# Optimization experiments

Hardware: AMD Instinct MI355X
Metric: run time of the kernel (lower is better)

Reference implementation:

```python
import jax, jax.numpy as jnp
import numpy as np

B, S, H, NH = 2, 2048, 768, 12
HD = H // NH
MEM_W = 0.5  # memory_weight
LN_EPS = 1e-5


def setup_inputs() -> dict:
    key = jax.random.key(0)
    ks = jax.random.split(key, 12)
    xav = lambda k: jax.random.uniform(k, (H, H), jnp.float32, -1.0, 1.0) * np.sqrt(6.0 / (H + H))
    return {
        "hidden_states": jax.random.normal(ks[0], (B, S, H), jnp.float32),
        "cross_states": jax.random.normal(ks[1], (B, S, H), jnp.float32),
        "attention_mask": jnp.ones((B, 1, S, S), jnp.int32),
        "memory_tensors": jax.random.normal(ks[2], (2, B, S, H), jnp.float32),
        "dynamic_factor": jax.random.uniform(ks[3], (B, S, 1), jnp.float32),
        "Wq": xav(ks[4]), "bq": jnp.zeros((H,), jnp.float32),
        "Wk": xav(ks[5]), "bk": jnp.zeros((H,), jnp.float32),
        "Wv": xav(ks[6]), "bv": jnp.zeros((H,), jnp.float32),
        "Wo": xav(ks[7]), "bo": jnp.zeros((H,), jnp.float32),
        "gate": jnp.ones((1,), jnp.float32),
        "gate_bias": jnp.zeros((1,), jnp.float32),
        "ln_g": jnp.ones((H,), jnp.float32),
        "ln_b": jnp.zeros((H,), jnp.float32),
    }


def _layernorm(x, g, b):
    mu = jnp.mean(x, axis=-1, keepdims=True)
    var = jnp.mean(jnp.square(x - mu), axis=-1, keepdims=True)
    return (x - mu) * jax.lax.rsqrt(var + LN_EPS) * g + b


def reference(hidden_states, cross_states, attention_mask, memory_tensors,
              dynamic_factor, Wq, bq, Wk, bk, Wv, bv, Wo, bo,
              gate, gate_bias, ln_g, ln_b):
    x = _layernorm(hidden_states, ln_g, ln_b)
    q = x @ Wq + bq                      # [B,S,H]
    k = cross_states @ Wk + bk
    v = cross_states @ Wv + bv
    k = k + memory_tensors[0] * MEM_W    # memory injection into K/V
    v = v + memory_tensors[1] * MEM_W

    q = q.reshape(B, S, NH, HD).transpose(0, 2, 1, 3)  # [B,NH,S,HD]
    k = k.reshape(B, S, NH, HD).transpose(0, 2, 1, 3)
    v = v.reshape(B, S, NH, HD).transpose(0, 2, 1, 3)

    scores = jnp.einsum("bhqd,bhkd->bhqk", q, k) / np.sqrt(HD)
    scores = jnp.where(attention_mask == 0, -jnp.inf, scores)
    attn = jax.nn.softmax(scores, axis=-1)
    out = jnp.einsum("bhqk,bhkd->bhqd", attn, v)       # [B,NH,S,HD]
    out = out.transpose(0, 2, 1, 3).reshape(B, S, H)

    out = out @ Wo + bo
    out = out * gate + gate_bias
    out = out * dynamic_factor
    return out
```

## Files before the change

kernel.cpp:

```cpp
#include <hip/hip_runtime.h>
#include <hip/hip_bf16.h>
#include <stdint.h>

#define BB   2
#define SS   2048
#define HH   768
#define NHH  12
#define HDD  64
#define BSS  (BB*SS)
#define NBH  (BB*NHH)
#define ROWS_BH (NBH*SS)
#define NSPLIT 2

typedef unsigned short u16;
typedef unsigned int   u32;
typedef __attribute__((ext_vector_type(8))) short bf16x8_t;
typedef __attribute__((ext_vector_type(4))) float f32x4;
typedef __attribute__((ext_vector_type(2))) u32   u32x2;
typedef __attribute__((ext_vector_type(4))) u32   u32x4;

#define MFMA16(a, b, c) __builtin_amdgcn_mfma_f32_16x16x32_bf16((a), (b), (c), 0, 0, 0)

__device__ __forceinline__ float b2f(u16 u) {
    u32 x = ((u32)u) << 16; float f; __builtin_memcpy(&f, &x, 4); return f;
}
__device__ __forceinline__ u16 f2b(float f) {
    u32 x; __builtin_memcpy(&x, &f, 4);
    u32 r = x + 0x7fffu + ((x >> 16) & 1u);
    return (u16)(r >> 16);
}
__device__ __forceinline__ void async16(const u16* g, u16* l) {
    __builtin_amdgcn_global_load_lds(
        (const __attribute__((address_space(1))) void*)g,
        (__attribute__((address_space(3))) void*)l, 16, 0, 0);
}

__global__ __launch_bounds__(256) void prep_kernel(
    const float* __restrict__ Wq, const float* __restrict__ Wk,
    const float* __restrict__ Wv, const float* __restrict__ Wo,
    u16* __restrict__ Wt,
    const float* __restrict__ hid, const float* __restrict__ cross,
    const float* __restrict__ g, const float* __restrict__ bb,
    u16* __restrict__ xln, u16* __restrict__ crossb,
    const int* __restrict__ mask, u32* __restrict__ bits,
    u32* __restrict__ wrow)
{
    int id = blockIdx.x;
    int t = threadIdx.x;

    if (id < 576) {
        int mat = id / 144, rem = id % 144;
        int by = rem / 12, bx = rem % 12;
        const float* src = (mat == 0) ? Wq : (mat == 1) ? Wk : (mat == 2) ? Wv : Wo;
        u16* dst = Wt + (size_t)mat * 768 * 768;

        __shared__ float sm[64][68];
        int r0 = by * 64, c0 = bx * 64;
        #pragma unroll
        for (int it = 0; it < 4; ++it) {
            int c = t + it * 256;
            int r = c >> 4, sg = c & 15;
            *(float4*)&sm[r][sg * 4] = *(const float4*)&src[(size_t)(r0 + r) * 768 + c0 + sg * 4];
        }
        __syncthreads();
        #pragma unroll
        for (int it = 0; it < 2; ++it) {
            int c = t + it * 256;
            int rr = c >> 3, sg = c & 7;
            u16 tmp[8] __attribute__((aligned(16)));
            #pragma unroll
            for (int j = 0; j < 8; ++j) tmp[j] = f2b(sm[sg * 8 + j][rr]);
            *(u32x4*)&dst[(size_t)(c0 + rr) * 768 + r0 + sg * 8] = *(u32x4*)tmp;
        }
        return;
    }

    if (id < 2624) {
        int lid = id - 576;
        int y = lid >> 10, bx = lid & 1023;
        int wv = t >> 6, lane = t & 63;
        int row = bx * 4 + wv;

        if (y == 1) {
            const float* xr = cross + (size_t)row * 768;
            u16* o = crossb + (size_t)row * 768;
            #pragma unroll
            for (int c = 0; c < 3; ++c) {
                float4 f = *(const float4*)&xr[c * 256 + lane * 4];
                u16 t4[4] __attribute__((aligned(8)));
                t4[0] = f2b(f.x); t4[1] = f2b(f.y); t4[2] = f2b(f.z); t4[3] = f2b(f.w);
                *(u32x2*)&o[c * 256 + lane * 4] = *(u32x2*)t4;
            }
            return;
        }

        const float* xr = hid + (size_t)row * 768;
        float v[12];
        float s = 0.f, s2 = 0.f;
        #pragma unroll
        for (int c = 0; c < 3; ++c) {
            float4 f = *(const float4*)&xr[c * 256 + lane * 4];
            v[c*4+0] = f.x; v[c*4+1] = f.y; v[c*4+2] = f.z; v[c*4+3] = f.w;
            s  += f.x + f.y + f.z + f.w;
            s2 += f.x*f.x + f.y*f.y + f.z*f.z + f.w*f.w;
        }
        #pragma unroll
        for (int off = 1; off < 64; off <<= 1) {
            s  += __shfl_xor(s,  off, 64);
            s2 += __shfl_xor(s2, off, 64);
        }
        float mu  = s  * (1.f / 768.f);
        float var = s2 * (1.f / 768.f) - mu * mu;
        float rs  = 1.f / sqrtf(var + 1e-5f);
        #pragma unroll
        for (int c = 0; c < 3; ++c) {
            float4 gg = *(const float4*)&g [c * 256 + lane * 4];
            float4 bv = *(const float4*)&bb[c * 256 + lane * 4];
            u16 o[4] __attribute__((aligned(8)));
            o[0] = f2b((v[c*4+0] - mu) * rs * gg.x + bv.x);
            o[1] = f2b((v[c*4+1] - mu) * rs * gg.y + bv.y);
            o[2] = f2b((v[c*4+2] - mu) * rs * gg.z + bv.z);
            o[3] = f2b((v[c*4+3] - mu) * rs * gg.w + bv.w);
            *(u32x2*)&xln[(size_t)row * 768 + c * 256 + lane * 4] = *(u32x2*)o;
        }
        return;
    }

    {
        int mid = id - 2624;
        int w = mid * 256 + t;
        const int4* p = (const int4*)(mask + (size_t)w * 32);
        u32 v = 0;
        #pragma unroll
        for (int i = 0; i < 8; ++i) {
            int4 m = p[i];
            v |= ((m.x != 0) ? 1u : 0u) << (4 * i + 0);
            v |= ((m.y != 0) ? 1u : 0u) << (4 * i + 1);
            v |= ((m.z != 0) ? 1u : 0u) << (4 * i + 2);
            v |= ((m.w != 0) ? 1u : 0u) << (4 * i + 3);
        }
        bits[w] = v;
        unsigned long long ball = __ballot(v == 0xffffffffu);
        if ((t & 63) == 0) {
            u32 wr = 0;
            #pragma unroll
            for (int kt = 0; kt < 32; ++kt)
                if (((ball >> (2 * kt)) & 3ull) == 3ull) wr |= (1u << kt);
            wrow[w >> 6] = wr;
        }
    }
}

__device__ __forceinline__ void gemm64_main(const u16* __restrict__ A,
                                            const u16* __restrict__ W,
                                            f32x4 acc[2][4])
{
    __shared__ __attribute__((aligned(16))) u16 AsL[64 * 64];
    __shared__ __attribute__((aligned(16))) u16 BsL[128 * 64];
    int m0 = blockIdx.x * 64, n0 = blockIdx.y * 128;
    int t = threadIdx.x;
    int wv = t >> 6, lane = t & 63, lm = lane & 15, quad = lane >> 4;
    int wr = wv >> 1, wc = wv & 1;

    for (int kt = 0; kt < 768 / 64; ++kt) {
        __syncthreads();
        #pragma unroll
        for (int it = 0; it < 2; ++it) {
            int c = t + it * 256;
            int row = c >> 3, cs = (c & 7) ^ (row & 7);
            async16(A + (size_t)(m0 + row) * 768 + kt * 64 + cs * 8, &AsL[c * 8]);
        }
        #pragma unroll
        for (int it = 0; it < 4; ++it) {
            int c = t + it * 256;
            int row = c >> 3, cs = (c & 7) ^ (row & 7);
            async16(W + (size_t)(n0 + row) * 768 + kt * 64 + cs * 8, &BsL[c * 8]);
        }
        __syncthreads();
        #pragma unroll
        for (int kk = 0; kk < 2; ++kk) {
            bf16x8_t af[2], bfv[4];
            #pragma unroll
            for (int i = 0; i < 2; ++i) {
                int r = wr * 32 + i * 16 + lm;
                af[i] = *(const bf16x8_t*)&AsL[(r * 8 + ((kk * 4 + quad) ^ (r & 7))) * 8];
            }
            #pragma unroll
            for (int j = 0; j < 4; ++j) {
                int r = wc * 64 + j * 16 + lm;
                bfv[j] = *(const bf16x8_t*)&BsL[(r * 8 + ((kk * 4 + quad) ^ (r & 7))) * 8];
            }
            #pragma unroll
            for (int i = 0; i < 2; ++i)
                #pragma unroll
                for (int j = 0; j < 4; ++j)
                    acc[i][j] = MFMA16(af[i], bfv[j], acc[i][j]);
        }
    }
}

__global__ __launch_bounds__(256) void qkv_gemm(
    const u16* __restrict__ xln, const u16* __restrict__ crossb,
    const u16* __restrict__ Wt,  const float* __restrict__ bq,
    const float* __restrict__ bk, const float* __restrict__ bv,
    const float* __restrict__ mem,
    u16* __restrict__ Qb, u16* __restrict__ Kb, u16* __restrict__ VtG)
{
    int z = blockIdx.z;
    const u16* A      = (z == 0) ? xln : crossb;
    const u16* W      = Wt + (size_t)z * 768 * 768;
    const float* bias = (z == 0) ? bq : (z == 1) ? bk : bv;
    const float* mp   = (z == 0) ? (const float*)nullptr : mem + (size_t)(z - 1) * BSS * HH;

    f32x4 z4 = {0.f, 0.f, 0.f, 0.f};
    f32x4 acc[2][4];
    #pragma unroll
    for (int i = 0; i < 2; ++i)
        #pragma unroll
        for (int j = 0; j < 4; ++j) acc[i][j] = z4;

    gemm64_main(A, W, acc);

    int t = threadIdx.x, wv = t >> 6, lane = t & 63, lm = lane & 15, quad = lane >> 4;
    int wr = wv >> 1, wc = wv & 1;
    int row0 = blockIdx.x * 64 + wr * 32 + quad * 4;
    int col0 = blockIdx.y * 128 + wc * 64 + lm;

    if (z == 2) {
        #pragma unroll
        for (int j = 0; j < 4; ++j) {
            int cg = col0 + j * 16;
            float bz = bias[cg];
            int h = cg >> 6, d = cg & 63;
            #pragma unroll
            for (int i = 0; i < 2; ++i) {
                int rg = row0 + i * 16;
                int b = rg >> 11, s = rg & 2047;
                u16 ob[4] __attribute__((aligned(8)));
                #pragma unroll
                for (int e = 0; e < 4; ++e) {
                    float v = acc[i][j][e] + bz + 0.5f * mp[(size_t)(rg + e) * HH + cg];
                    ob[e] = f2b(v);
                }
                *(u32x2*)&VtG[((size_t)(b * NHH + h) * 64 + d) * SS + s] = *(u32x2*)ob;
            }
        }
        return;
    }

    u16* out = (z == 0) ? Qb : Kb;
    #pragma unroll
    for (int j = 0; j < 4; ++j) {
        int cg = col0 + j * 16;
        float bz = bias[cg];
        #pragma unroll
        for (int i = 0; i < 2; ++i) {
            int rg = row0 + i * 16;
            #pragma unroll
            for (int e = 0; e < 4; ++e) {
                float v = acc[i][j][e] + bz;
                if (mp) v += 0.5f * mp[(size_t)(rg + e) * HH + cg];
                out[(size_t)(rg + e) * HH + cg] = f2b(v);
            }
        }
    }
}

__global__ __launch_bounds__(512) void attn_kernel(
    const u16* __restrict__ Q, const u16* __restrict__ K,
    const u16* __restrict__ VtG, const u32* __restrict__ mbits,
    const u32* __restrict__ wrow,
    u16* __restrict__ Pacc, float* __restrict__ Pl, int ksteps)
{
    __shared__ __attribute__((aligned(16))) u16   KsL[2][64 * 64];
    __shared__ __attribute__((aligned(16))) u16   VtL[2][64 * 64];
    __shared__ __attribute__((aligned(16))) short Ps[8][16][72];

    int qt = blockIdx.x;
    int bh = blockIdx.y;
    int z  = blockIdx.z;
    int b = bh / NHH, h = bh % NHH;
    int t = threadIdx.x;
    int wv = t >> 6, lane = t & 63, lm = lane & 15, quad = lane >> 4;
    int r7 = lm & 7;

    int qrow_g = b * SS + qt * 128 + wv * 16;
    const u16* qp = Q + (size_t)(qrow_g + lm) * HH + h * 64;
    bf16x8_t qf0 = *(const bf16x8_t*)&qp[quad * 8];
    bf16x8_t qf1 = *(const bf16x8_t*)&qp[32 + quad * 8];

    f32x4 z4 = {0.f, 0.f, 0.f, 0.f};
    f32x4 acc_o[4] = {z4, z4, z4, z4};
    float l_part[4] = {0.f, 0.f, 0.f, 0.f};

    const float SC = 0.18033688011112042f;
    int qloc = qt * 128 + wv * 16 + quad * 4;

    u32 wand = wrow[b * SS + qloc + 0] & wrow[b * SS + qloc + 1] &
               wrow[b * SS + qloc + 2] & wrow[b * SS + qloc + 3];

    int kr = t >> 3, cs = (t & 7) ^ (kr & 7);
    const u16* Kb0 = K + (size_t)(b * SS) * HH + h * 64;
    const u16* Vb0 = VtG + (size_t)bh * 64 * SS;

    auto STAGE = [&](int pp, int kt) {
        int k0 = kt * 64;
        async16(Kb0 + (size_t)(k0 + kr) * HH + cs * 8, &KsL[pp][t * 8]);
        async16(Vb0 + (size_t)kr * SS + k0 + cs * 8,   &VtL[pp][t * 8]);
    };

    int kt0 = z * ksteps, ktE = kt0 + ksteps;
    STAGE(0, kt0);
    __syncthreads();

    for (int kt = kt0; kt < ktE; ++kt) {
        int p = (kt - kt0) & 1;
        if (kt + 1 < ktE) STAGE(p ^ 1, kt + 1);

        f32x4 sc[4];
        #pragma unroll
        for (int k16 = 0; k16 < 4; ++k16) {
            int rowk = k16 * 16 + lm;
            bf16x8_t kf0 = *(const bf16x8_t*)&KsL[p][(rowk * 8 + (quad ^ r7)) * 8];
            bf16x8_t kf1 = *(const bf16x8_t*)&KsL[p][(rowk * 8 + ((quad ^ 4) ^ r7)) * 8];
            f32x4 a = z4;
            a = MFMA16(qf0, kf0, a);
            a = MFMA16(qf1, kf1, a);
            sc[k16] = a;
        }

        if (!__all((int)((wand >> kt) & 1u))) {
            #pragma unroll
            for (int e = 0; e < 4; ++e) {
                u32x2 u = *(const u32x2*)&mbits[(size_t)(b * SS + qloc + e) * (SS / 32) + kt * 2];
                unsigned long long mw = ((unsigned long long)u.y << 32) | (unsigned long long)u.x;
                #pragma unroll
                for (int k16 = 0; k16 < 4; ++k16)
                    if (!((mw >> (k16 * 16 + lm)) & 1ull)) sc[k16][e] = -3.0e38f;
            }
        }

        #pragma unroll
        for (int k16 = 0; k16 < 4; ++k16) {
            #pragma unroll
            for (int e = 0; e < 4; ++e) {
                float pv = __builtin_amdgcn_exp2f(sc[k16][e] * SC);
                sc[k16][e] = pv;
                l_part[e] += pv;
            }
        }

        #pragma unroll
        for (int k16 = 0; k16 < 4; ++k16) {
            int colg = ((k16 + quad) & 3) * 16;
            #pragma unroll
            for (int e = 0; e < 4; ++e) {
                float pv = sc[k16][e];
                u32 pb = __builtin_bit_cast(u32, pv);
                Ps[wv][quad * 4 + e][colg + lm] = (short)((pb + 0x8000u) >> 16);
            }
        }
        __asm__ volatile("" ::: "memory");

        #pragma unroll
        for (int cc = 0; cc < 2; ++cc) {
            int k16r = cc * 2 + (quad >> 1);
            int colg = ((k16r + (lm >> 2)) & 3) * 16 + (quad & 1) * 8;
            bf16x8_t pf = *(const bf16x8_t*)&Ps[wv][lm][colg];
            #pragma unroll
            for (int j = 0; j < 4; ++j) {
                bf16x8_t vf = *(const bf16x8_t*)&VtL[p][((j * 16 + lm) * 8 + ((cc * 4 + quad) ^ r7)) * 8];
                acc_o[j] = MFMA16(pf, vf, acc_o[j]);
            }
        }

        __syncthreads();
    }

    #pragma unroll
    for (int off = 1; off < 16; off <<= 1) {
        #pragma unroll
        for (int e = 0; e < 4; ++e)
            l_part[e] += __shfl_xor(l_part[e], off, 64);
    }

    size_t prow = ((size_t)z * NBH + bh) * SS + qt * 128 + wv * 16 + quad * 4;
    #pragma unroll
    for (int j = 0; j < 4; ++j)
        #pragma unroll
        for (int e = 0; e < 4; ++e)
            Pacc[(prow + e) * 64 + j * 16 + lm] = f2b(acc_o[j][e]);
    if (lm == 0) {
        #pragma unroll
        for (int e = 0; e < 4; ++e)
            Pl[prow + e] = l_part[e];
    }
}

__global__ __launch_bounds__(256) void attn_merge(
    const u16* __restrict__ Pacc, const float* __restrict__ Pl,
    u16* __restrict__ AO)
{
    int t = threadIdx.x;
    int r = blockIdx.x * 64 + (t >> 2);
    int dseg = (t & 3) * 16;

    float lsum = Pl[r] + Pl[(size_t)ROWS_BH + r];

    float o[16];
    #pragma unroll
    for (int i = 0; i < 16; ++i) o[i] = 0.f;
    #pragma unroll
    for (int s = 0; s < NSPLIT; ++s) {
        const u16* ap = &Pacc[((size_t)s * ROWS_BH + r) * 64 + dseg];
        u32x4 a0 = *(const u32x4*)ap;
        u32x4 a1 = *(const u32x4*)(ap + 8);
        u32 wa[8];
        wa[0]=a0.x; wa[1]=a0.y; wa[2]=a0.z; wa[3]=a0.w;
        wa[4]=a1.x; wa[5]=a1.y; wa[6]=a1.z; wa[7]=a1.w;
        #pragma unroll
        for (int i = 0; i < 8; ++i) {
            o[2*i]   += b2f((u16)(wa[i] & 0xffff));
            o[2*i+1] += b2f((u16)(wa[i] >> 16));
        }
    }
    float inv = 1.f / lsum;
    int bh = r >> 11, q = r & 2047;
    int b = bh / NHH, h = bh % NHH;
    u16 ob[16] __attribute__((aligned(16)));
    #pragma unroll
    for (int i = 0; i < 16; ++i) ob[i] = f2b(o[i] * inv);
    u16* op = &AO[((size_t)(b * SS + q)) * HH + h * 64 + dseg];
    *(u32x4*)op       = *(u32x4*)ob;
    *(u32x4*)(op + 8) = *(u32x4*)(ob + 8);
}

__global__ __launch_bounds__(256) void out_gemm(
    const u16* __restrict__ AO, const u16* __restrict__ Wt,
    const float* __restrict__ bo, const float* __restrict__ gate,
    const float* __restrict__ gbias, const float* __restrict__ dyn,
    float* __restrict__ out)
{
    f32x4 z4 = {0.f, 0.f, 0.f, 0.f};
    f32x4 acc[2][4];
    #pragma unroll
    for (int i = 0; i < 2; ++i)
        #pragma unroll
        for (int j = 0; j < 4; ++j) acc[i][j] = z4;

    gemm64_main(AO, Wt, acc);

    float gv = gate[0];
    float gb = gbias[0];
    int t = threadIdx.x, wv = t >> 6, lane = t & 63, lm = lane & 15, quad = lane >> 4;
    int wr = wv >> 1, wc = wv & 1;
    int row0 = blockIdx.x * 64 + wr * 32 + quad * 4;
    int col0 = blockIdx.y * 128 + wc * 64 + lm;
    #pragma unroll
    for (int j = 0; j < 4; ++j) {
        int cg = col0 + j * 16;
        float bz = bo[cg];
        #pragma unroll
        for (int i = 0; i < 2; ++i) {
            int rg = row0 + i * 16;
            #pragma unroll
            for (int e = 0; e < 4; ++e) {
                float v = acc[i][j][e] + bz;
                v = v * gv + gb;
                v *= dyn[rg + e];
                out[(size_t)(rg + e) * HH + cg] = v;
            }
        }
    }
}

extern "C" void kernel_launch(void* const* d_in, const int* in_sizes, int n_in,
                              void* d_out, int out_size, void* d_ws, size_t ws_size,
                              hipStream_t stream)
{
    (void)in_sizes; (void)n_in; (void)out_size; (void)ws_size;

    const float* hid   = (const float*)d_in[0];
    const float* cross = (const float*)d_in[1];
    const int*   amask = (const int*)d_in[2];
    const float* mem   = (const float*)d_in[3];
    const float* dyn   = (const float*)d_in[4];
    const float* Wq    = (const float*)d_in[5];
    const float* bq    = (const float*)d_in[6];
    const float* Wk    = (const float*)d_in[7];
    const float* bk    = (const float*)d_in[8];
    const float* Wv    = (const float*)d_in[9];
    const float* bv    = (const float*)d_in[10];
    const float* Wo    = (const float*)d_in[11];
    const float* bo    = (const float*)d_in[12];
    const float* gate  = (const float*)d_in[13];
    const float* gbias = (const float*)d_in[14];
    const float* lng   = (const float*)d_in[15];
    const float* lnb   = (const float*)d_in[16];

    char* p = (char*)d_ws;
    u16* Wt   = (u16*)p; p += (size_t)4 * 768 * 768 * 2;
    u32* mb   = (u32*)p; p += (size_t)BB * SS * (SS / 32) * 4;
    u32* wrow = (u32*)p; p += (size_t)BSS * 4;
    u16* xln  = (u16*)p; p += (size_t)BSS * HH * 2;
    u16* crb  = (u16*)p; p += (size_t)BSS * HH * 2;
    u16* Qb   = (u16*)p; p += (size_t)BSS * HH * 2;
    u16* Kb   = (u16*)p; p += (size_t)BSS * HH * 2;
    u16* VtG  = (u16*)p; p += (size_t)BSS * HH * 2;
    u16* Pacc  = xln;
    float* Pl  = (float*)Wt;
    u16* AO    = Kb;

    prep_kernel <<<dim3(3648),           256, 0, stream>>>(
        Wq, Wk, Wv, Wo, Wt, hid, cross, lng, lnb, xln, crb, amask, mb, wrow);
    qkv_gemm    <<<dim3(64, 6, 3),       256, 0, stream>>>(
        xln, crb, Wt, bq, bk, bv, mem, Qb, Kb, VtG);
    attn_kernel <<<dim3(16, 24, NSPLIT), 512, 0, stream>>>(
        Qb, Kb, VtG, mb, wrow, Pacc, Pl, SS / 64 / NSPLIT);
    attn_merge  <<<dim3(ROWS_BH / 64),   256, 0, stream>>>(Pacc, Pl, AO);
    out_gemm    <<<dim3(64, 6),          256, 0, stream>>>(
        AO, Wt + (size_t)3 * 768 * 768, bo, gate, gbias, dyn, (float*)d_out);
}
```

Measured before the change: 246.3 us.

## Process two 16-row query tiles per wave in attention, halving block size

The attention kernel now uses 256 threads (4 waves), and each wave handles 32 query rows as two 16-row MFMA tiles instead of one. Each K and V fragment read from LDS is reused for two MFMAs, which cuts LDS read traffic per FLOP. The staging loop copies two chunks per thread to fill the same 64x64 tiles. The cost is roughly double the accumulator and score registers per thread; the launch bound asks for 3 blocks per CU to keep occupancy.

```diff
diff --git a/kernel.cpp b/kernel.cpp
--- a/kernel.cpp
+++ b/kernel.cpp
@@ -266,7 +266,7 @@
     }
 }
 
-__global__ __launch_bounds__(512) void attn_kernel(
+__global__ __launch_bounds__(256, 3) void attn_kernel(
     const u16* __restrict__ Q, const u16* __restrict__ K,
     const u16* __restrict__ VtG, const u32* __restrict__ mbits,
     const u32* __restrict__ wrow,
@@ -274,7 +274,7 @@
 {
     __shared__ __attribute__((aligned(16))) u16   KsL[2][64 * 64];
     __shared__ __attribute__((aligned(16))) u16   VtL[2][64 * 64];
-    __shared__ __attribute__((aligned(16))) short Ps[8][16][72];
+    __shared__ __attribute__((aligned(16))) short Ps[4][32][72];
 
     int qt = blockIdx.x;
     int bh = blockIdx.y;
@@ -284,29 +284,42 @@
     int wv = t >> 6, lane = t & 63, lm = lane & 15, quad = lane >> 4;
     int r7 = lm & 7;
 
-    int qrow_g = b * SS + qt * 128 + wv * 16;
-    const u16* qp = Q + (size_t)(qrow_g + lm) * HH + h * 64;
-    bf16x8_t qf0 = *(const bf16x8_t*)&qp[quad * 8];
-    bf16x8_t qf1 = *(const bf16x8_t*)&qp[32 + quad * 8];
+    int qrow0 = b * SS + qt * 128 + wv * 32;
+    const u16* qp0 = Q + (size_t)(qrow0 + lm) * HH + h * 64;
+    const u16* qp1 = Q + (size_t)(qrow0 + 16 + lm) * HH + h * 64;
+    bf16x8_t qa0 = *(const bf16x8_t*)&qp0[quad * 8];
+    bf16x8_t qa1 = *(const bf16x8_t*)&qp0[32 + quad * 8];
+    bf16x8_t qb0 = *(const bf16x8_t*)&qp1[quad * 8];
+    bf16x8_t qb1 = *(const bf16x8_t*)&qp1[32 + quad * 8];
 
     f32x4 z4 = {0.f, 0.f, 0.f, 0.f};
-    f32x4 acc_o[4] = {z4, z4, z4, z4};
-    float l_part[4] = {0.f, 0.f, 0.f, 0.f};
+    f32x4 acc0[4] = {z4, z4, z4, z4};
+    f32x4 acc1[4] = {z4, z4, z4, z4};
+    float l0[4] = {0.f, 0.f, 0.f, 0.f};
+    float l1[4] = {0.f, 0.f, 0.f, 0.f};
 
     const float SC = 0.18033688011112042f;
-    int qloc = qt * 128 + wv * 16 + quad * 4;
-
-    u32 wand = wrow[b * SS + qloc + 0] & wrow[b * SS + qloc + 1] &
-               wrow[b * SS + qloc + 2] & wrow[b * SS + qloc + 3];
-
-    int kr = t >> 3, cs = (t & 7) ^ (kr & 7);
+    int ql0 = qt * 128 + wv * 32 + quad * 4;
+    int ql1 = ql0 + 16;
+
+    u32 wand0 = wrow[b * SS + ql0 + 0] & wrow[b * SS + ql0 + 1] &
+                wrow[b * SS + ql0 + 2] & wrow[b * SS + ql0 + 3];
+    u32 wand1 = wrow[b * SS + ql1 + 0] & wrow[b * SS + ql1 + 1] &
+                wrow[b * SS + ql1 + 2] & wrow[b * SS + ql1 + 3];
+    u32 wandA = wand0 & wand1;
+
     const u16* Kb0 = K + (size_t)(b * SS) * HH + h * 64;
     const u16* Vb0 = VtG + (size_t)bh * 64 * SS;
 
     auto STAGE = [&](int pp, int kt) {
         int k0 = kt * 64;
-        async16(Kb0 + (size_t)(k0 + kr) * HH + cs * 8, &KsL[pp][t * 8]);
-        async16(Vb0 + (size_t)kr * SS + k0 + cs * 8,   &VtL[pp][t * 8]);
+        #pragma unroll
+        for (int it = 0; it < 2; ++it) {
+            int c = t + it * 256;
+            int kr = c >> 3, cs = (c & 7) ^ (kr & 7);
+            async16(Kb0 + (size_t)(k0 + kr) * HH + cs * 8, &KsL[pp][c * 8]);
+            async16(Vb0 + (size_t)kr * SS + k0 + cs * 8,   &VtL[pp][c * 8]);
+        }
     };
 
     int kt0 = z * ksteps, ktE = kt0 + ksteps;
@@ -317,36 +330,33 @@
         int p = (kt - kt0) & 1;
         if (kt + 1 < ktE) STAGE(p ^ 1, kt + 1);
 
-        f32x4 sc[4];
+        f32x4 sc0[4], sc1[4];
         #pragma unroll
         for (int k16 = 0; k16 < 4; ++k16) {
             int rowk = k16 * 16 + lm;
             bf16x8_t kf0 = *(const bf16x8_t*)&KsL[p][(rowk * 8 + (quad ^ r7)) * 8];
             bf16x8_t kf1 = *(const bf16x8_t*)&KsL[p][(rowk * 8 + ((quad ^ 4) ^ r7)) * 8];
-            f32x4 a = z4;
-            a = MFMA16(qf0, kf0, a);
-            a = MFMA16(qf1, kf1, a);
-            sc[k16] = a;
-        }
-
-        if (!__all((int)((wand >> kt) & 1u))) {
+            f32x4 a0 = z4, a1 = z4;
+            a0 = MFMA16(qa0, kf0, a0);
+            a1 = MFMA16(qb0, kf0, a1);
+            a0 = MFMA16(qa1, kf1, a0);
+            a1 = MFMA16(qb1, kf1, a1);
+            sc0[k16] = a0;
+            sc1[k16] = a1;
+        }
+
+        if (!__all((int)((wandA >> kt) & 1u))) {
             #pragma unroll
             for (int e = 0; e < 4; ++e) {
-                u32x2 u = *(const u32x2*)&mbits[(size_t)(b * SS + qloc + e) * (SS / 32) + kt * 2];
-                unsigned long long mw = ((unsigned long long)u.y << 32) | (unsigned long long)u.x;
+                u32x2 u0 = *(const u32x2*)&mbits[(size_t)(b * SS + ql0 + e) * (SS / 32) + kt * 2];
+                unsigned long long mw0 = ((unsigned long long)u0.y << 32) | (unsigned long long)u0.x;
+                u32x2 u1 = *(const u32x2*)&mbits[(size_t)(b * SS + ql1 + e) * (SS / 32) + kt * 2];
+                unsigned long long mw1 = ((unsigned long long)u1.y << 32) | (unsigned long long)u1.x;
                 #pragma unroll
-                for (int k16 = 0; k16 < 4; ++k16)
-                    if (!((mw >> (k16 * 16 + lm)) & 1ull)) sc[k16][e] = -3.0e38f;
-            }
-        }
-
-        #pragma unroll
-        for (int k16 = 0; k16 < 4; ++k16) {
-            #pragma unroll
-            for (int e = 0; e < 4; ++e) {
-                float pv = __builtin_amdgcn_exp2f(sc[k16][e] * SC);
-                sc[k16][e] = pv;
-                l_part[e] += pv;
+                for (int k16 = 0; k16 < 4; ++k16) {
+                    if (!((mw0 >> (k16 * 16 + lm)) & 1ull)) sc0[k16][e] = -3.0e38f;
+                    if (!((mw1 >> (k16 * 16 + lm)) & 1ull)) sc1[k16][e] = -3.0e38f;
+                }
             }
         }
 
@@ -355,9 +365,14 @@
             int colg = ((k16 + quad) & 3) * 16;
             #pragma unroll
             for (int e = 0; e < 4; ++e) {
-                float pv = sc[k16][e];
-                u32 pb = __builtin_bit_cast(u32, pv);
-                Ps[wv][quad * 4 + e][colg + lm] = (short)((pb + 0x8000u) >> 16);
+                float p0 = __builtin_amdgcn_exp2f(sc0[k16][e] * SC);
+                float p1 = __builtin_amdgcn_exp2f(sc1[k16][e] * SC);
+                l0[e] += p0;
+                l1[e] += p1;
+                u32 pb0 = __builtin_bit_cast(u32, p0);
+                u32 pb1 = __builtin_bit_cast(u32, p1);
+                Ps[wv][quad * 4 + e][colg + lm]      = (short)((pb0 + 0x8000u) >> 16);
+                Ps[wv][16 + quad * 4 + e][colg + lm] = (short)((pb1 + 0x8000u) >> 16);
             }
         }
         __asm__ volatile("" ::: "memory");
@@ -366,11 +381,13 @@
         for (int cc = 0; cc < 2; ++cc) {
             int k16r = cc * 2 + (quad >> 1);
             int colg = ((k16r + (lm >> 2)) & 3) * 16 + (quad & 1) * 8;
-            bf16x8_t pf = *(const bf16x8_t*)&Ps[wv][lm][colg];
+            bf16x8_t pf0 = *(const bf16x8_t*)&Ps[wv][lm][colg];
+            bf16x8_t pf1 = *(const bf16x8_t*)&Ps[wv][16 + lm][colg];
             #pragma unroll
             for (int j = 0; j < 4; ++j) {
                 bf16x8_t vf = *(const bf16x8_t*)&VtL[p][((j * 16 + lm) * 8 + ((cc * 4 + quad) ^ r7)) * 8];
-                acc_o[j] = MFMA16(pf, vf, acc_o[j]);
+                acc0[j] = MFMA16(pf0, vf, acc0[j]);
+                acc1[j] = MFMA16(pf1, vf, acc1[j]);
             }
         }
 
@@ -380,20 +397,27 @@
     #pragma unroll
     for (int off = 1; off < 16; off <<= 1) {
         #pragma unroll
-        for (int e = 0; e < 4; ++e)
-            l_part[e] += __shfl_xor(l_part[e], off, 64);
-    }
-
-    size_t prow = ((size_t)z * NBH + bh) * SS + qt * 128 + wv * 16 + quad * 4;
+        for (int e = 0; e < 4; ++e) {
+            l0[e] += __shfl_xor(l0[e], off, 64);
+            l1[e] += __shfl_xor(l1[e], off, 64);
+        }
+    }
+
+    size_t prow0 = ((size_t)z * NBH + bh) * SS + qt * 128 + wv * 32 + quad * 4;
+    size_t prow1 = prow0 + 16;
     #pragma unroll
     for (int j = 0; j < 4; ++j)
         #pragma unroll
-        for (int e = 0; e < 4; ++e)
-            Pacc[(prow + e) * 64 + j * 16 + lm] = f2b(acc_o[j][e]);
+        for (int e = 0; e < 4; ++e) {
+            Pacc[(prow0 + e) * 64 + j * 16 + lm] = f2b(acc0[j][e]);
+            Pacc[(prow1 + e) * 64 + j * 16 + lm] = f2b(acc1[j][e]);
+        }
     if (lm == 0) {
         #pragma unroll
-        for (int e = 0; e < 4; ++e)
-            Pl[prow + e] = l_part[e];
+        for (int e = 0; e < 4; ++e) {
+            Pl[prow0 + e] = l0[e];
+            Pl[prow1 + e] = l1[e];
+        }
     }
 }
 
@@ -515,7 +539,7 @@
         Wq, Wk, Wv, Wo, Wt, hid, cross, lng, lnb, xln, crb, amask, mb, wrow);
     qkv_gemm    <<<dim3(64, 6, 3),       256, 0, stream>>>(
         xln, crb, Wt, bq, bk, bv, mem, Qb, Kb, VtG);
-    attn_kernel <<<dim3(16, 24, NSPLIT), 512, 0, stream>>>(
+    attn_kernel <<<dim3(16, 24, NSPLIT), 256, 0, stream>>>(
         Qb, Kb, VtG, mb, wrow, Pacc, Pl, SS / 64 / NSPLIT);
     attn_merge  <<<dim3(ROWS_BH / 64),   256, 0, stream>>>(Pacc, Pl, AO);
     out_gemm    <<<dim3(64, 6),          256, 0, stream>>>(
```

Result: faster. 240.5 us (-2.3%).

## Rewrite attention inner loop with 32x32 MFMA and register-resident P via permlane swap

Applied to the files above, without the earlier changes.

Switches the attention kernel from 16x16x32 MFMA tiles to 32x32x16 tiles, computing S^T = K·Q^T so each wave owns 32 query rows, and keeps the softmax probabilities in registers. It converts them with packed bf16 conversion and a permlane32 swap instead of round-tripping through LDS. Blocks shrink to 256 threads with a min-occupancy hint of 3, and each thread stages two K/V chunks. Masking is now applied after the exp by zeroing probabilities. The intent is to cut LDS traffic and the instruction count per tile, at the cost of higher register pressure from the 16-wide accumulators.

```diff
diff --git a/kernel.cpp b/kernel.cpp
--- a/kernel.cpp
+++ b/kernel.cpp
@@ -16,10 +16,12 @@
 typedef unsigned int   u32;
 typedef __attribute__((ext_vector_type(8))) short bf16x8_t;
 typedef __attribute__((ext_vector_type(4))) float f32x4;
+typedef __attribute__((ext_vector_type(16))) float f32x16;
 typedef __attribute__((ext_vector_type(2))) u32   u32x2;
 typedef __attribute__((ext_vector_type(4))) u32   u32x4;
 
 #define MFMA16(a, b, c) __builtin_amdgcn_mfma_f32_16x16x32_bf16((a), (b), (c), 0, 0, 0)
+#define MFMA32(a, b, c) __builtin_amdgcn_mfma_f32_32x32x16_bf16((a), (b), (c), 0, 0, 0)
 
 __device__ __forceinline__ float b2f(u16 u) {
     u32 x = ((u32)u) << 16; float f; __builtin_memcpy(&f, &x, 4); return f;
@@ -28,6 +30,11 @@
     u32 x; __builtin_memcpy(&x, &f, 4);
     u32 r = x + 0x7fffu + ((x >> 16) & 1u);
     return (u16)(r >> 16);
+}
+__device__ __forceinline__ u32 cvtpk(float a, float b) {
+    u32 r;
+    __asm__("v_cvt_pk_bf16_f32 %0, %1, %2" : "=v"(r) : "v"(a), "v"(b));
+    return r;
 }
 __device__ __forceinline__ void async16(const u16* g, u16* l) {
     __builtin_amdgcn_global_load_lds(
@@ -266,38 +273,38 @@
     }
 }
 
-__global__ __launch_bounds__(512) void attn_kernel(
+__global__ __launch_bounds__(256, 3) void attn_kernel(
     const u16* __restrict__ Q, const u16* __restrict__ K,
     const u16* __restrict__ VtG, const u32* __restrict__ mbits,
     const u32* __restrict__ wrow,
     u16* __restrict__ Pacc, float* __restrict__ Pl, int ksteps)
 {
-    __shared__ __attribute__((aligned(16))) u16   KsL[2][64 * 64];
-    __shared__ __attribute__((aligned(16))) u16   VtL[2][64 * 64];
-    __shared__ __attribute__((aligned(16))) short Ps[8][16][72];
+    __shared__ __attribute__((aligned(16))) u16 KsL[2][64 * 64];
+    __shared__ __attribute__((aligned(16))) u16 VtL[2][64 * 64];
 
     int qt = blockIdx.x;
     int bh = blockIdx.y;
     int z  = blockIdx.z;
     int b = bh / NHH, h = bh % NHH;
     int t = threadIdx.x;
-    int wv = t >> 6, lane = t & 63, lm = lane & 15, quad = lane >> 4;
-    int r7 = lm & 7;
-
-    int qrow_g = b * SS + qt * 128 + wv * 16;
-    const u16* qp = Q + (size_t)(qrow_g + lm) * HH + h * 64;
-    bf16x8_t qf0 = *(const bf16x8_t*)&qp[quad * 8];
-    bf16x8_t qf1 = *(const bf16x8_t*)&qp[32 + quad * 8];
-
-    f32x4 z4 = {0.f, 0.f, 0.f, 0.f};
-    f32x4 acc_o[4] = {z4, z4, z4, z4};
-    float l_part[4] = {0.f, 0.f, 0.f, 0.f};
+    int wv = t >> 6, lane = t & 63;
+    int q31 = lane & 31, hi = lane >> 5;
+
+    int qbase = qt * 128 + wv * 32;
+    const u16* qp = Q + (size_t)(b * SS + qbase + q31) * HH + h * 64 + hi * 8;
+    bf16x8_t qf0 = *(const bf16x8_t*)&qp[0];
+    bf16x8_t qf1 = *(const bf16x8_t*)&qp[16];
+    bf16x8_t qf2 = *(const bf16x8_t*)&qp[32];
+    bf16x8_t qf3 = *(const bf16x8_t*)&qp[48];
+
+    f32x16 acc0 = {};
+    f32x16 acc1 = {};
+    float l_lane = 0.f;
 
     const float SC = 0.18033688011112042f;
-    int qloc = qt * 128 + wv * 16 + quad * 4;
-
-    u32 wand = wrow[b * SS + qloc + 0] & wrow[b * SS + qloc + 1] &
-               wrow[b * SS + qloc + 2] & wrow[b * SS + qloc + 3];
+
+    u32 wl = wrow[b * SS + qbase + q31];
+    const u32* mrow = &mbits[(size_t)(b * SS + qbase + q31) * (SS / 32)];
 
     int kr = t >> 3, cs = (t & 7) ^ (kr & 7);
     const u16* Kb0 = K + (size_t)(b * SS) * HH + h * 64;
@@ -305,9 +312,15 @@
 
     auto STAGE = [&](int pp, int kt) {
         int k0 = kt * 64;
-        async16(Kb0 + (size_t)(k0 + kr) * HH + cs * 8, &KsL[pp][t * 8]);
-        async16(Vb0 + (size_t)kr * SS + k0 + cs * 8,   &VtL[pp][t * 8]);
+        #pragma unroll
+        for (int it = 0; it < 2; ++it) {
+            int c = t + it * 256;
+            int rr = c >> 3, ss = (c & 7) ^ (rr & 7);
+            async16(Kb0 + (size_t)(k0 + rr) * HH + ss * 8, &KsL[pp][c * 8]);
+            async16(Vb0 + (size_t)rr * SS + k0 + ss * 8,   &VtL[pp][c * 8]);
+        }
     };
+    (void)kr; (void)cs;
 
     int kt0 = z * ksteps, ktE = kt0 + ksteps;
     STAGE(0, kt0);
@@ -317,84 +330,72 @@
         int p = (kt - kt0) & 1;
         if (kt + 1 < ktE) STAGE(p ^ 1, kt + 1);
 
-        f32x4 sc[4];
-        #pragma unroll
-        for (int k16 = 0; k16 < 4; ++k16) {
-            int rowk = k16 * 16 + lm;
-            bf16x8_t kf0 = *(const bf16x8_t*)&KsL[p][(rowk * 8 + (quad ^ r7)) * 8];
-            bf16x8_t kf1 = *(const bf16x8_t*)&KsL[p][(rowk * 8 + ((quad ^ 4) ^ r7)) * 8];
-            f32x4 a = z4;
-            a = MFMA16(qf0, kf0, a);
-            a = MFMA16(qf1, kf1, a);
-            sc[k16] = a;
-        }
-
-        if (!__all((int)((wand >> kt) & 1u))) {
-            #pragma unroll
-            for (int e = 0; e < 4; ++e) {
-                u32x2 u = *(const u32x2*)&mbits[(size_t)(b * SS + qloc + e) * (SS / 32) + kt * 2];
-                unsigned long long mw = ((unsigned long long)u.y << 32) | (unsigned long long)u.x;
-                #pragma unroll
-                for (int k16 = 0; k16 < 4; ++k16)
-                    if (!((mw >> (k16 * 16 + lm)) & 1ull)) sc[k16][e] = -3.0e38f;
-            }
-        }
-
-        #pragma unroll
-        for (int k16 = 0; k16 < 4; ++k16) {
-            #pragma unroll
-            for (int e = 0; e < 4; ++e) {
-                float pv = __builtin_amdgcn_exp2f(sc[k16][e] * SC);
-                sc[k16][e] = pv;
-                l_part[e] += pv;
-            }
-        }
-
-        #pragma unroll
-        for (int k16 = 0; k16 < 4; ++k16) {
-            int colg = ((k16 + quad) & 3) * 16;
-            #pragma unroll
-            for (int e = 0; e < 4; ++e) {
-                float pv = sc[k16][e];
-                u32 pb = __builtin_bit_cast(u32, pv);
-                Ps[wv][quad * 4 + e][colg + lm] = (short)((pb + 0x8000u) >> 16);
-            }
-        }
-        __asm__ volatile("" ::: "memory");
-
-        #pragma unroll
-        for (int cc = 0; cc < 2; ++cc) {
-            int k16r = cc * 2 + (quad >> 1);
-            int colg = ((k16r + (lm >> 2)) & 3) * 16 + (quad & 1) * 8;
-            bf16x8_t pf = *(const bf16x8_t*)&Ps[wv][lm][colg];
-            #pragma unroll
-            for (int j = 0; j < 4; ++j) {
-                bf16x8_t vf = *(const bf16x8_t*)&VtL[p][((j * 16 + lm) * 8 + ((cc * 4 + quad) ^ r7)) * 8];
-                acc_o[j] = MFMA16(pf, vf, acc_o[j]);
+        bool ok = __all((int)((wl >> kt) & 1u));
+        unsigned long long mw = ~0ull;
+        if (!ok) {
+            u32x2 u = *(const u32x2*)&mrow[kt * 2];
+            mw = ((unsigned long long)u.y << 32) | (unsigned long long)u.x;
+        }
+
+        #pragma unroll
+        for (int kb = 0; kb < 2; ++kb) {
+            f32x16 sc = {};
+            #pragma unroll
+            for (int step = 0; step < 4; ++step) {
+                int row = kb * 32 + q31;
+                int ch = (step * 2 + hi) ^ (row & 7);
+                bf16x8_t kf = *(const bf16x8_t*)&KsL[p][(row * 8 + ch) * 8];
+                bf16x8_t qf = (step == 0) ? qf0 : (step == 1) ? qf1 : (step == 2) ? qf2 : qf3;
+                sc = MFMA32(kf, qf, sc);
+            }
+
+            #pragma unroll
+            for (int r = 0; r < 16; ++r) {
+                float pv = __builtin_amdgcn_exp2f(sc[r] * SC);
+                if (!ok) {
+                    int kbit = kb * 32 + (r & 3) + 8 * (r >> 2) + 4 * hi;
+                    if (!((mw >> kbit) & 1ull)) pv = 0.f;
+                }
+                sc[r] = pv;
+                l_lane += pv;
+            }
+
+            #pragma unroll
+            for (int s2 = 0; s2 < 2; ++s2) {
+                u32 P0 = cvtpk(sc[8 * s2 + 0], sc[8 * s2 + 1]);
+                u32 P1 = cvtpk(sc[8 * s2 + 2], sc[8 * s2 + 3]);
+                u32 P2 = cvtpk(sc[8 * s2 + 4], sc[8 * s2 + 5]);
+                u32 P3 = cvtpk(sc[8 * s2 + 6], sc[8 * s2 + 7]);
+                auto s02 = __builtin_amdgcn_permlane32_swap((int)P0, (int)P2, false, false);
+                auto s13 = __builtin_amdgcn_permlane32_swap((int)P1, (int)P3, false, false);
+                u32x4 w;
+                w.x = (u32)s02[0]; w.y = (u32)s13[0];
+                w.z = (u32)s02[1]; w.w = (u32)s13[1];
+                bf16x8_t pf = __builtin_bit_cast(bf16x8_t, w);
+
+                int vrow0 = q31;
+                int vrow1 = 32 + q31;
+                int ch = kb * 4 + s2 * 2 + hi;
+                bf16x8_t vf0 = *(const bf16x8_t*)&VtL[p][(vrow0 * 8 + (ch ^ (vrow0 & 7))) * 8];
+                bf16x8_t vf1 = *(const bf16x8_t*)&VtL[p][(vrow1 * 8 + (ch ^ (vrow1 & 7))) * 8];
+                acc0 = MFMA32(pf, vf0, acc0);
+                acc1 = MFMA32(pf, vf1, acc1);
             }
         }
 
         __syncthreads();
     }
 
-    #pragma unroll
-    for (int off = 1; off < 16; off <<= 1) {
-        #pragma unroll
-        for (int e = 0; e < 4; ++e)
-            l_part[e] += __shfl_xor(l_part[e], off, 64);
-    }
-
-    size_t prow = ((size_t)z * NBH + bh) * SS + qt * 128 + wv * 16 + quad * 4;
-    #pragma unroll
-    for (int j = 0; j < 4; ++j)
-        #pragma unroll
-        for (int e = 0; e < 4; ++e)
-            Pacc[(prow + e) * 64 + j * 16 + lm] = f2b(acc_o[j][e]);
-    if (lm == 0) {
-        #pragma unroll
-        for (int e = 0; e < 4; ++e)
-            Pl[prow + e] = l_part[e];
-    }
+    l_lane += __shfl_xor(l_lane, 32, 64);
+
+    size_t prow0 = ((size_t)z * NBH + bh) * SS + qt * 128 + wv * 32;
+    #pragma unroll
+    for (int r = 0; r < 16; ++r) {
+        int qrow = (r & 3) + 8 * (r >> 2) + 4 * hi;
+        Pacc[(prow0 + qrow) * 64 + q31]      = f2b(acc0[r]);
+        Pacc[(prow0 + qrow) * 64 + 32 + q31] = f2b(acc1[r]);
+    }
+    if (lane < 32) Pl[prow0 + lane] = l_lane;
 }
 
 __global__ __launch_bounds__(256) void attn_merge(
@@ -515,7 +516,7 @@
         Wq, Wk, Wv, Wo, Wt, hid, cross, lng, lnb, xln, crb, amask, mb, wrow);
     qkv_gemm    <<<dim3(64, 6, 3),       256, 0, stream>>>(
         xln, crb, Wt, bq, bk, bv, mem, Qb, Kb, VtG);
-    attn_kernel <<<dim3(16, 24, NSPLIT), 512, 0, stream>>>(
+    attn_kernel <<<dim3(16, 24, NSPLIT), 256, 0, stream>>>(
         Qb, Kb, VtG, mb, wrow, Pacc, Pl, SS / 64 / NSPLIT);
     attn_merge  <<<dim3(ROWS_BH / 64),   256, 0, stream>>>(Pacc, Pl, AO);
     out_gemm    <<<dim3(64, 6),          256, 0, stream>>>(
```

Result: faster. 238.7 us (-3.1%).
